# Optimization experiments

Measured on AMD Instinct MI355X. Metric: run time of the kernel, lower is better.

Reference implementation:

```python
import jax, jax.numpy as jnp
import numpy as np

EPS = 1e-5  # torch GroupNorm default


def setup_inputs() -> dict:
    key = jax.random.key(0)
    k1, k2, k3 = jax.random.split(key, 3)
    bs, l, dim = 16, 2048, 512
    G, varDim, numCodes = 2, 256, 320
    x = jax.random.normal(k1, (bs, l, dim), dtype=jnp.float32)
    # grouped 1x1 Conv1d weight: (groups, out_per_group, in_per_group)
    proj_w = jax.random.normal(k2, (G, varDim, varDim), dtype=jnp.float32) / np.sqrt(varDim)
    gn_weight = jnp.ones((dim,), dtype=jnp.float32)
    gn_bias = jnp.zeros((dim,), dtype=jnp.float32)
    embeddings = 0.01 * jax.random.normal(k3, (numCodes, 1, varDim), dtype=jnp.float32)
    return {"x": x, "proj_w": proj_w, "gn_weight": gn_weight,
            "gn_bias": gn_bias, "embeddings": embeddings}


def reference(x, proj_w, gn_weight, gn_bias, embeddings):
    bs, l, dim = x.shape
    G, varDim, _ = proj_w.shape
    numCodes = embeddings.shape[0]

    # --- projection: grouped 1x1 conv ---
    xg = x.transpose(0, 2, 1).reshape(bs, G, varDim, l)            # (bs,G,v,l)
    ze_g = jnp.einsum('gov,bgvl->bgol', proj_w, xg)                # (bs,G,v,l)

    # --- Fp32GroupNorm over (C/G * L) per group ---
    zf = ze_g.astype(jnp.float32)
    mean = zf.mean(axis=(2, 3), keepdims=True)
    var = zf.var(axis=(2, 3), keepdims=True)
    zn = (zf - mean) * jax.lax.rsqrt(var + EPS)
    ze = zn.reshape(bs, dim, l) * gn_weight[None, :, None] + gn_bias[None, :, None]
    ze = ze.astype(x.dtype)                                        # (bs,dim,l)

    # --- VQ: nearest code per group (argmin of L2 == argmin of sq dist) ---
    z = ze.reshape(bs, G, varDim, l).transpose(0, 3, 1, 2)         # (bs,l,G,v)
    emb = jnp.broadcast_to(embeddings, (numCodes, G, varDim))      # combineGroups expand
    dots = jnp.einsum('blgv,cgv->blgc', z, emb)                    # (bs,l,G,C)
    e2 = jnp.sum(emb * emb, axis=-1)                               # (C,G)
    dist = e2.T[None, None] - 2.0 * dots                           # ||z||^2 dropped: const over C
    idx = jnp.argmin(dist, axis=-1)                                # (bs,l,G)

    # gather codes per group
    zq = jnp.take_along_axis(
        emb.transpose(1, 0, 2)[None, None],                        # (1,1,G,C,v)
        idx[..., None, None], axis=3).squeeze(3)                   # (bs,l,G,v)
    zq = zq.reshape(bs, l, dim)

    # straight-through estimator; output shape (bs, l, dim)
    ze_bld = ze.transpose(0, 2, 1)
    out = jax.lax.stop_gradient(zq) + ze_bld - jax.lax.stop_gradient(ze_bld)
    return out
```

## Files before the change

### kernel.cpp

```cpp
#include <hip/hip_runtime.h>
#include <math.h>

typedef _Float16 half8_t  __attribute__((ext_vector_type(8)));
typedef _Float16 half4_t  __attribute__((ext_vector_type(4)));
typedef float    floatx16 __attribute__((ext_vector_type(16)));

#define BS   16
#define LL   2048
#define DIMC 512
#define NG   2
#define VD   256
#define NC   320
#define NELEM ((double)(VD*LL))

#define GLL(gsrc, ldst) __builtin_amdgcn_global_load_lds( \
    (const __attribute__((address_space(1))) unsigned int*)(gsrc), \
    (__attribute__((address_space(3))) unsigned int*)(ldst), 16, 0, 0)

#define MFMA32 __builtin_amdgcn_mfma_f32_32x32x16_f16

__global__ void k_prep(const float* __restrict__ W, const float* __restrict__ emb,
                       _Float16* __restrict__ Wimg, _Float16* __restrict__ Eimg,
                       float* __restrict__ e2f)
{
  const int blk = blockIdx.x, t = threadIdx.x;
  if (blk < 64) {
    int base = (blk * 256 + t) * 8;
    int k = base & 255, c = k >> 5, kk = k & 31;
    int row = (base >> 8) & 255, g = base >> 16;
    float4 v0 = *(const float4*)(W + base);
    float4 v1 = *(const float4*)(W + base + 4);
    float vv[8] = {v0.x, v0.y, v0.z, v0.w, v1.x, v1.y, v1.z, v1.w};
    half8_t hh, ll;
    #pragma unroll
    for (int i = 0; i < 8; ++i) {
      float s = vv[i] * 16.0f;
      _Float16 h = (_Float16)s;
      hh[i] = h; ll[i] = (_Float16)(s - (float)h);
    }
    size_t rb = ((size_t)(g * 8 + c) * 256 + row) * 72;
    *(half8_t*)&Wimg[rb + kk]      = hh;
    *(half8_t*)&Wimg[rb + 32 + kk] = ll;
  } else if (blk < 104) {
    int base = ((blk - 64) * 256 + t) * 8;
    int k = base & 255, c = k >> 5, kk = k & 31;
    int code = base >> 8;
    float4 v0 = *(const float4*)(emb + base);
    float4 v1 = *(const float4*)(emb + base + 4);
    float vv[8] = {v0.x, v0.y, v0.z, v0.w, v1.x, v1.y, v1.z, v1.w};
    half8_t hh, ll;
    #pragma unroll
    for (int i = 0; i < 8; ++i) {
      float s = vv[i] * 64.0f;
      _Float16 h = (_Float16)s;
      hh[i] = h; ll[i] = (_Float16)(s - (float)h);
    }
    size_t rb = ((size_t)c * 320 + code) * 72;
    *(half8_t*)&Eimg[rb + kk]      = hh;
    *(half8_t*)&Eimg[rb + 32 + kk] = ll;
  } else {
    int code = (blk - 104) * 256 + t;
    if (code < NC) {
      const float* er = emb + (size_t)code * VD;
      double s[4] = {0.0, 0.0, 0.0, 0.0};
      for (int v = 0; v < VD; v += 16)
        #pragma unroll
        for (int u = 0; u < 4; ++u) {
          float4 e4 = *(const float4*)(er + v + u * 4);
          s[u] += (double)e4.x * e4.x + (double)e4.y * e4.y
                + (double)e4.z * e4.z + (double)e4.w * e4.w;
        }
      e2f[code] = (float)(64.0 * (s[0] + s[1] + s[2] + s[3]));
    }
  }
}

__global__ __launch_bounds__(256, 2) void k_proj(
    const float* __restrict__ x, const _Float16* __restrict__ Wimg,
    float* __restrict__ ze, double* __restrict__ stats)
{
  __shared__ _Float16 Ah[128][72];
  __shared__ _Float16 Bh[256 * 72];

  const int blk = blockIdx.x;
  const int g  = blk & 1;
  const int m0 = (blk >> 1) * 128;
  const int b  = m0 >> 11;
  const int t  = threadIdx.x;
  const int lane = t & 63, w = t >> 6;
  const int col  = lane & 31, hq = lane >> 5;
  const int mw = (w & 1) * 64, nw = (w >> 1) * 128;

  const char* wbase = (const char*)(Wimg + (size_t)g * 8 * 256 * 72);

  floatx16 acc[2][4];
  #pragma unroll
  for (int i = 0; i < 2; ++i)
    #pragma unroll
    for (int j = 0; j < 4; ++j)
      #pragma unroll
      for (int e = 0; e < 16; ++e) acc[i][j][e] = 0.f;

  for (int c = 0; c < 8; ++c) {
    {
      const char* wc = wbase + (size_t)c * 256 * 144;
      #pragma unroll
      for (int i = 0; i < 9; ++i) {
        int off = (w * 9 + i) * 1024 + lane * 16;
        GLL(wc + off, (char*)Bh + off);
      }
    }
    #pragma unroll
    for (int i = 0; i < 4; ++i) {
      int idx = i * 256 + t;
      int row = idx >> 3, kq = idx & 7;
      float4 v = *(const float4*)(x + ((size_t)(m0 + row)) * DIMC + g * VD + c * 32 + kq * 4);
      half4_t hh, ll;
      { _Float16 h = (_Float16)v.x; hh[0] = h; ll[0] = (_Float16)(v.x - (float)h); }
      { _Float16 h = (_Float16)v.y; hh[1] = h; ll[1] = (_Float16)(v.y - (float)h); }
      { _Float16 h = (_Float16)v.z; hh[2] = h; ll[2] = (_Float16)(v.z - (float)h); }
      { _Float16 h = (_Float16)v.w; hh[3] = h; ll[3] = (_Float16)(v.w - (float)h); }
      *(half4_t*)&Ah[row][kq * 4]      = hh;
      *(half4_t*)&Ah[row][32 + kq * 4] = ll;
    }
    __syncthreads();
    #pragma unroll
    for (int ks = 0; ks < 2; ++ks) {
      const int ko = ks * 16 + hq * 8;
      half8_t azh[2], azl[2], bwh[4], bwl[4];
      #pragma unroll
      for (int i = 0; i < 2; ++i) {
        azh[i] = *(const half8_t*)&Ah[mw + i * 32 + col][ko];
        azl[i] = *(const half8_t*)&Ah[mw + i * 32 + col][32 + ko];
      }
      #pragma unroll
      for (int j = 0; j < 4; ++j) {
        bwh[j] = *(const half8_t*)&Bh[(nw + j * 32 + col) * 72 + ko];
        bwl[j] = *(const half8_t*)&Bh[(nw + j * 32 + col) * 72 + 32 + ko];
      }
      #pragma unroll
      for (int mi = 0; mi < 2; ++mi)
        #pragma unroll
        for (int ni = 0; ni < 4; ++ni) {
          acc[mi][ni] = MFMA32(azh[mi], bwh[ni], acc[mi][ni], 0, 0, 0);
          acc[mi][ni] = MFMA32(azh[mi], bwl[ni], acc[mi][ni], 0, 0, 0);
          acc[mi][ni] = MFMA32(azl[mi], bwh[ni], acc[mi][ni], 0, 0, 0);
        }
    }
    __syncthreads();
  }

  double s1 = 0.0, s2 = 0.0;
  #pragma unroll
  for (int mi = 0; mi < 2; ++mi)
    #pragma unroll
    for (int ni = 0; ni < 4; ++ni)
      #pragma unroll
      for (int r = 0; r < 16; ++r) {
        float vv = acc[mi][ni][r] * 0.0625f;
        double d = (double)vv; s1 += d; s2 += d * d;
        int ml = mw + mi * 32 + (r & 3) + 8 * (r >> 2) + 4 * hq;
        int nl = nw + ni * 32 + col;
        ze[((size_t)(m0 + ml)) * DIMC + g * VD + nl] = vv;
      }
  #pragma unroll
  for (int off = 32; off > 0; off >>= 1) {
    s1 += __shfl_down(s1, off);
    s2 += __shfl_down(s2, off);
  }
  if (lane == 0) {
    atomicAdd(&stats[(b * NG + g) * 2 + 0], s1);
    atomicAdd(&stats[(b * NG + g) * 2 + 1], s2);
  }
}

__global__ __launch_bounds__(256, 2) void k_vq(
    float* __restrict__ zio, const float* __restrict__ emb,
    const _Float16* __restrict__ Eimg,
    const float* __restrict__ gnw, const float* __restrict__ gnb,
    const double* __restrict__ stats, const float* __restrict__ e2f)
{
  __shared__ _Float16 Zs[128][72];
  __shared__ _Float16 Es[320 * 72];
  __shared__ float e2sh[NC];
  __shared__ int   idxs[128];
  __shared__ float cndv[2][128];
  __shared__ int   cndi[2][128];

  const int blk = blockIdx.x;
  const int g  = blk & 1;
  const int m0 = (blk >> 1) * 128;
  const int b  = m0 >> 11;
  const int t  = threadIdx.x;
  const int lane = t & 63, w = t >> 6;
  const int col  = lane & 31, hq = lane >> 5;
  const int ph = w & 1;
  const int mh = w >> 1;

  const int si = b * NG + g;
  double ss1 = stats[2 * si], ss2 = stats[2 * si + 1];
  double mu = ss1 / NELEM, var = ss2 / NELEM - mu * mu;
  const float mean = (float)mu;
  const float rstd = (float)(1.0 / sqrt(var + 1e-5));

  for (int c = t; c < NC; c += 256) e2sh[c] = e2f[c];

  float* zbase = zio + (size_t)m0 * DIMC + g * VD;
  const float* gw = gnw + g * VD;
  const float* gb = gnb + g * VD;

  floatx16 acc[5][2];
  #pragma unroll
  for (int i = 0; i < 5; ++i)
    #pragma unroll
    for (int f = 0; f < 2; ++f)
      #pragma unroll
      for (int e = 0; e < 16; ++e) acc[i][f][e] = 0.f;

  for (int c = 0; c < 8; ++c) {
    {
      const char* ec = (const char*)Eimg + (size_t)c * 320 * 144;
      for (int i = w; i < 45; i += 4) {
        int off = i * 1024 + lane * 16;
        GLL(ec + off, (char*)Es + off);
      }
    }
    #pragma unroll
    for (int i = 0; i < 4; ++i) {
      int idx = i * 256 + t;
      int row = idx >> 3, kq = idx & 7;
      float4 v  = *(const float4*)(zbase + (size_t)row * DIMC + c * 32 + kq * 4);
      float4 w4 = *(const float4*)(gw + c * 32 + kq * 4);
      float4 b4 = *(const float4*)(gb + c * 32 + kq * 4);
      float zn0 = (v.x - mean) * rstd * w4.x + b4.x;
      float zn1 = (v.y - mean) * rstd * w4.y + b4.y;
      float zn2 = (v.z - mean) * rstd * w4.z + b4.z;
      float zn3 = (v.w - mean) * rstd * w4.w + b4.w;
      half4_t hh, ll;
      { _Float16 h = (_Float16)zn0; hh[0] = h; ll[0] = (_Float16)(zn0 - (float)h); }
      { _Float16 h = (_Float16)zn1; hh[1] = h; ll[1] = (_Float16)(zn1 - (float)h); }
      { _Float16 h = (_Float16)zn2; hh[2] = h; ll[2] = (_Float16)(zn2 - (float)h); }
      { _Float16 h = (_Float16)zn3; hh[3] = h; ll[3] = (_Float16)(zn3 - (float)h); }
      *(half4_t*)&Zs[row][kq * 4]      = hh;
      *(half4_t*)&Zs[row][32 + kq * 4] = ll;
    }
    __syncthreads();
    #pragma unroll
    for (int ks = 0; ks < 2; ++ks) {
      const int ko = ks * 16 + hq * 8;
      half8_t bzh[2], bzl[2];
      #pragma unroll
      for (int f = 0; f < 2; ++f) {
        bzh[f] = *(const half8_t*)&Zs[ph * 64 + f * 32 + col][ko];
        bzl[f] = *(const half8_t*)&Zs[ph * 64 + f * 32 + col][32 + ko];
      }
      #pragma unroll
      for (int mtl = 0; mtl < 5; ++mtl) {
        const _Float16* erow = &Es[((mh * 5 + mtl) * 32 + col) * 72];
        half8_t aeh = *(const half8_t*)&erow[ko];
        half8_t ael = *(const half8_t*)&erow[32 + ko];
        #pragma unroll
        for (int f = 0; f < 2; ++f) {
          acc[mtl][f] = MFMA32(aeh, bzh[f], acc[mtl][f], 0, 0, 0);
          acc[mtl][f] = MFMA32(aeh, bzl[f], acc[mtl][f], 0, 0, 0);
          acc[mtl][f] = MFMA32(ael, bzh[f], acc[mtl][f], 0, 0, 0);
        }
      }
    }
    __syncthreads();
  }

  float bv0 = 3.4e38f, bv1 = 3.4e38f;
  int   bi0 = 0x7fffffff, bi1 = 0x7fffffff;
  #pragma unroll
  for (int mtl = 0; mtl < 5; ++mtl)
    #pragma unroll
    for (int r = 0; r < 16; ++r) {
      int code = (mh * 5 + mtl) * 32 + (r & 3) + 8 * (r >> 2) + 4 * hq;
      float d0 = e2sh[code] - 2.0f * acc[mtl][0][r];
      if (d0 < bv0 || (d0 == bv0 && code < bi0)) { bv0 = d0; bi0 = code; }
      float d1 = e2sh[code] - 2.0f * acc[mtl][1][r];
      if (d1 < bv1 || (d1 == bv1 && code < bi1)) { bv1 = d1; bi1 = code; }
    }
  {
    float ov = __shfl_xor(bv0, 32); int oi = __shfl_xor(bi0, 32);
    if (ov < bv0 || (ov == bv0 && oi < bi0)) { bv0 = ov; bi0 = oi; }
    ov = __shfl_xor(bv1, 32); oi = __shfl_xor(bi1, 32);
    if (ov < bv1 || (ov == bv1 && oi < bi1)) { bv1 = ov; bi1 = oi; }
  }
  if (hq == 0) {
    cndv[mh][ph * 64 + col]      = bv0; cndi[mh][ph * 64 + col]      = bi0;
    cndv[mh][ph * 64 + 32 + col] = bv1; cndi[mh][ph * 64 + 32 + col] = bi1;
  }
  __syncthreads();
  if (t < 128) {
    float v0 = cndv[0][t], v1 = cndv[1][t];
    int   i0 = cndi[0][t], i1 = cndi[1][t];
    idxs[t] = (v1 < v0 || (v1 == v0 && i1 < i0)) ? i1 : i0;
  }
  __syncthreads();

  #pragma unroll
  for (int it = 0; it < 32; ++it) {
    int idx = it * 256 + t;
    int row = idx >> 6, q4 = (idx & 63) * 4;
    int id = idxs[row];
    float4 e4 = *(const float4*)(emb + (size_t)id * VD + q4);
    *(float4*)(zbase + (size_t)row * DIMC + q4) = e4;
  }
}

extern "C" void kernel_launch(void* const* d_in, const int* in_sizes, int n_in,
                              void* d_out, int out_size, void* d_ws, size_t ws_size,
                              hipStream_t stream) {
  const float* x   = (const float*)d_in[0];
  const float* W   = (const float*)d_in[1];
  const float* gnw = (const float*)d_in[2];
  const float* gnb = (const float*)d_in[3];
  const float* emb = (const float*)d_in[4];
  float* out = (float*)d_out;

  double*   stats = (double*)d_ws;
  float*    e2f   = (float*)((char*)d_ws + 512);
  _Float16* Wimg  = (_Float16*)((char*)d_ws + 2048);
  _Float16* Eimg  = (_Float16*)((char*)d_ws + 591872);

  hipMemsetAsync(d_ws, 0, 512, stream);
  k_prep<<<106, 256, 0, stream>>>(W, emb, Wimg, Eimg, e2f);
  k_proj<<<512, 256, 0, stream>>>(x, Wimg, out, stats);
  k_vq<<<512, 256, 0, stream>>>(out, emb, Eimg, gnw, gnb, stats, e2f);
}
```

Measured before the change: 197.0 us.

## Double-buffer LDS tiles and use 512-thread blocks in proj and VQ kernels

After: 230.4 us. 16.9% more time.

```diff
diff --git a/kernel.cpp b/kernel.cpp
--- a/kernel.cpp
+++ b/kernel.cpp
@@ -75,12 +75,12 @@
   }
 }
 
-__global__ __launch_bounds__(256, 2) void k_proj(
+__global__ __launch_bounds__(512, 1) void k_proj(
     const float* __restrict__ x, const _Float16* __restrict__ Wimg,
     float* __restrict__ ze, double* __restrict__ stats)
 {
-  __shared__ _Float16 Ah[128][72];
-  __shared__ _Float16 Bh[256 * 72];
+  __shared__ _Float16 Ah[2][128][72];
+  __shared__ _Float16 Bh[2][256 * 72];
 
   const int blk = blockIdx.x;
   const int g  = blk & 1;
@@ -89,78 +89,99 @@
   const int t  = threadIdx.x;
   const int lane = t & 63, w = t >> 6;
   const int col  = lane & 31, hq = lane >> 5;
-  const int mw = (w & 1) * 64, nw = (w >> 1) * 128;
+  const int pw = (w & 1) * 64, ow = (w >> 1) * 64;
+  const int rw = t >> 3, kq = t & 7;
 
   const char* wbase = (const char*)(Wimg + (size_t)g * 8 * 256 * 72);
-
-  floatx16 acc[2][4];
+  const float* xrow = x + (size_t)m0 * DIMC + g * VD + kq * 4;
+
+  floatx16 acc[2][2];
   #pragma unroll
   for (int i = 0; i < 2; ++i)
     #pragma unroll
-    for (int j = 0; j < 4; ++j)
+    for (int j = 0; j < 2; ++j)
       #pragma unroll
       for (int e = 0; e < 16; ++e) acc[i][j][e] = 0.f;
 
+  for (int i = w; i < 36; i += 8) {
+    int off = i * 1024 + lane * 16;
+    GLL(wbase + off, (char*)Bh[0] + off);
+  }
+  #pragma unroll
+  for (int i = 0; i < 2; ++i) {
+    int row = i * 64 + rw;
+    float4 v = *(const float4*)(xrow + (size_t)row * DIMC);
+    half4_t hh, ll;
+    { _Float16 h = (_Float16)v.x; hh[0] = h; ll[0] = (_Float16)(v.x - (float)h); }
+    { _Float16 h = (_Float16)v.y; hh[1] = h; ll[1] = (_Float16)(v.y - (float)h); }
+    { _Float16 h = (_Float16)v.z; hh[2] = h; ll[2] = (_Float16)(v.z - (float)h); }
+    { _Float16 h = (_Float16)v.w; hh[3] = h; ll[3] = (_Float16)(v.w - (float)h); }
+    *(half4_t*)&Ah[0][row][kq * 4]      = hh;
+    *(half4_t*)&Ah[0][row][32 + kq * 4] = ll;
+  }
+
   for (int c = 0; c < 8; ++c) {
-    {
-      const char* wc = wbase + (size_t)c * 256 * 144;
-      #pragma unroll
-      for (int i = 0; i < 9; ++i) {
-        int off = (w * 9 + i) * 1024 + lane * 16;
-        GLL(wc + off, (char*)Bh + off);
-      }
-    }
-    #pragma unroll
-    for (int i = 0; i < 4; ++i) {
-      int idx = i * 256 + t;
-      int row = idx >> 3, kq = idx & 7;
-      float4 v = *(const float4*)(x + ((size_t)(m0 + row)) * DIMC + g * VD + c * 32 + kq * 4);
-      half4_t hh, ll;
-      { _Float16 h = (_Float16)v.x; hh[0] = h; ll[0] = (_Float16)(v.x - (float)h); }
-      { _Float16 h = (_Float16)v.y; hh[1] = h; ll[1] = (_Float16)(v.y - (float)h); }
-      { _Float16 h = (_Float16)v.z; hh[2] = h; ll[2] = (_Float16)(v.z - (float)h); }
-      { _Float16 h = (_Float16)v.w; hh[3] = h; ll[3] = (_Float16)(v.w - (float)h); }
-      *(half4_t*)&Ah[row][kq * 4]      = hh;
-      *(half4_t*)&Ah[row][32 + kq * 4] = ll;
-    }
     __syncthreads();
+    const int cur = c & 1, nxt = cur ^ 1;
+    if (c < 7) {
+      const char* wc = wbase + (size_t)(c + 1) * 256 * 144;
+      for (int i = w; i < 36; i += 8) {
+        int off = i * 1024 + lane * 16;
+        GLL(wc + off, (char*)Bh[nxt] + off);
+      }
+    }
+    float4 xv[2];
+    if (c < 7) {
+      #pragma unroll
+      for (int i = 0; i < 2; ++i)
+        xv[i] = *(const float4*)(xrow + (size_t)(i * 64 + rw) * DIMC + (c + 1) * 32);
+    }
     #pragma unroll
     for (int ks = 0; ks < 2; ++ks) {
       const int ko = ks * 16 + hq * 8;
-      half8_t azh[2], azl[2], bwh[4], bwl[4];
+      half8_t azh[2], azl[2], bwh[2], bwl[2];
       #pragma unroll
       for (int i = 0; i < 2; ++i) {
-        azh[i] = *(const half8_t*)&Ah[mw + i * 32 + col][ko];
-        azl[i] = *(const half8_t*)&Ah[mw + i * 32 + col][32 + ko];
-      }
-      #pragma unroll
-      for (int j = 0; j < 4; ++j) {
-        bwh[j] = *(const half8_t*)&Bh[(nw + j * 32 + col) * 72 + ko];
-        bwl[j] = *(const half8_t*)&Bh[(nw + j * 32 + col) * 72 + 32 + ko];
+        azh[i] = *(const half8_t*)&Ah[cur][pw + i * 32 + col][ko];
+        azl[i] = *(const half8_t*)&Ah[cur][pw + i * 32 + col][32 + ko];
+        bwh[i] = *(const half8_t*)&Bh[cur][(ow + i * 32 + col) * 72 + ko];
+        bwl[i] = *(const half8_t*)&Bh[cur][(ow + i * 32 + col) * 72 + 32 + ko];
       }
       #pragma unroll
       for (int mi = 0; mi < 2; ++mi)
         #pragma unroll
-        for (int ni = 0; ni < 4; ++ni) {
+        for (int ni = 0; ni < 2; ++ni) {
           acc[mi][ni] = MFMA32(azh[mi], bwh[ni], acc[mi][ni], 0, 0, 0);
           acc[mi][ni] = MFMA32(azh[mi], bwl[ni], acc[mi][ni], 0, 0, 0);
           acc[mi][ni] = MFMA32(azl[mi], bwh[ni], acc[mi][ni], 0, 0, 0);
         }
     }
-    __syncthreads();
+    if (c < 7) {
+      #pragma unroll
+      for (int i = 0; i < 2; ++i) {
+        int row = i * 64 + rw;
+        half4_t hh, ll;
+        { _Float16 h = (_Float16)xv[i].x; hh[0] = h; ll[0] = (_Float16)(xv[i].x - (float)h); }
+        { _Float16 h = (_Float16)xv[i].y; hh[1] = h; ll[1] = (_Float16)(xv[i].y - (float)h); }
+        { _Float16 h = (_Float16)xv[i].z; hh[2] = h; ll[2] = (_Float16)(xv[i].z - (float)h); }
+        { _Float16 h = (_Float16)xv[i].w; hh[3] = h; ll[3] = (_Float16)(xv[i].w - (float)h); }
+        *(half4_t*)&Ah[nxt][row][kq * 4]      = hh;
+        *(half4_t*)&Ah[nxt][row][32 + kq * 4] = ll;
+      }
+    }
   }
 
   double s1 = 0.0, s2 = 0.0;
   #pragma unroll
   for (int mi = 0; mi < 2; ++mi)
     #pragma unroll
-    for (int ni = 0; ni < 4; ++ni)
+    for (int ni = 0; ni < 2; ++ni)
       #pragma unroll
       for (int r = 0; r < 16; ++r) {
         float vv = acc[mi][ni][r] * 0.0625f;
         double d = (double)vv; s1 += d; s2 += d * d;
-        int ml = mw + mi * 32 + (r & 3) + 8 * (r >> 2) + 4 * hq;
-        int nl = nw + ni * 32 + col;
+        int ml = pw + mi * 32 + (r & 3) + 8 * (r >> 2) + 4 * hq;
+        int nl = ow + ni * 32 + col;
         ze[((size_t)(m0 + ml)) * DIMC + g * VD + nl] = vv;
       }
   #pragma unroll
@@ -174,14 +195,14 @@
   }
 }
 
-__global__ __launch_bounds__(256, 2) void k_vq(
+__global__ __launch_bounds__(512, 1) void k_vq(
     float* __restrict__ zio, const float* __restrict__ emb,
     const _Float16* __restrict__ Eimg,
     const float* __restrict__ gnw, const float* __restrict__ gnb,
     const double* __restrict__ stats, const float* __restrict__ e2f)
 {
-  __shared__ _Float16 Zs[128][72];
-  __shared__ _Float16 Es[320 * 72];
+  __shared__ _Float16 Zs[2][128][72];
+  __shared__ _Float16 Es[2][320 * 72];
   __shared__ float e2sh[NC];
   __shared__ int   idxs[128];
   __shared__ float cndv[2][128];
@@ -194,8 +215,9 @@
   const int t  = threadIdx.x;
   const int lane = t & 63, w = t >> 6;
   const int col  = lane & 31, hq = lane >> 5;
-  const int ph = w & 1;
-  const int mh = w >> 1;
+  const int ph = (w & 3) * 32;
+  const int mh = (w >> 2) * 5;
+  const int rw = t >> 3, kq = t & 7;
 
   const int si = b * NG + g;
   double ss1 = stats[2 * si], ss2 = stats[2 * si + 1];
@@ -203,94 +225,112 @@
   const float mean = (float)mu;
   const float rstd = (float)(1.0 / sqrt(var + 1e-5));
 
-  for (int c = t; c < NC; c += 256) e2sh[c] = e2f[c];
+  for (int cc = t; cc < NC; cc += 512) e2sh[cc] = e2f[cc];
 
   float* zbase = zio + (size_t)m0 * DIMC + g * VD;
+  const float* zrow = zbase + kq * 4;
   const float* gw = gnw + g * VD;
   const float* gb = gnb + g * VD;
 
-  floatx16 acc[5][2];
+  floatx16 acc[5];
   #pragma unroll
   for (int i = 0; i < 5; ++i)
     #pragma unroll
-    for (int f = 0; f < 2; ++f)
-      #pragma unroll
-      for (int e = 0; e < 16; ++e) acc[i][f][e] = 0.f;
-
-  for (int c = 0; c < 8; ++c) {
-    {
-      const char* ec = (const char*)Eimg + (size_t)c * 320 * 144;
-      for (int i = w; i < 45; i += 4) {
-        int off = i * 1024 + lane * 16;
-        GLL(ec + off, (char*)Es + off);
-      }
-    }
-    #pragma unroll
-    for (int i = 0; i < 4; ++i) {
-      int idx = i * 256 + t;
-      int row = idx >> 3, kq = idx & 7;
-      float4 v  = *(const float4*)(zbase + (size_t)row * DIMC + c * 32 + kq * 4);
-      float4 w4 = *(const float4*)(gw + c * 32 + kq * 4);
-      float4 b4 = *(const float4*)(gb + c * 32 + kq * 4);
-      float zn0 = (v.x - mean) * rstd * w4.x + b4.x;
-      float zn1 = (v.y - mean) * rstd * w4.y + b4.y;
-      float zn2 = (v.z - mean) * rstd * w4.z + b4.z;
-      float zn3 = (v.w - mean) * rstd * w4.w + b4.w;
+    for (int e = 0; e < 16; ++e) acc[i][e] = 0.f;
+
+  for (int i = w; i < 45; i += 8) {
+    int off = i * 1024 + lane * 16;
+    GLL((const char*)Eimg + off, (char*)Es[0] + off);
+  }
+  {
+    float4 wv = *(const float4*)(gw + kq * 4);
+    float4 bv = *(const float4*)(gb + kq * 4);
+    #pragma unroll
+    for (int i = 0; i < 2; ++i) {
+      int row = i * 64 + rw;
+      float4 v = *(const float4*)(zrow + (size_t)row * DIMC);
+      float zn0 = (v.x - mean) * rstd * wv.x + bv.x;
+      float zn1 = (v.y - mean) * rstd * wv.y + bv.y;
+      float zn2 = (v.z - mean) * rstd * wv.z + bv.z;
+      float zn3 = (v.w - mean) * rstd * wv.w + bv.w;
       half4_t hh, ll;
       { _Float16 h = (_Float16)zn0; hh[0] = h; ll[0] = (_Float16)(zn0 - (float)h); }
       { _Float16 h = (_Float16)zn1; hh[1] = h; ll[1] = (_Float16)(zn1 - (float)h); }
       { _Float16 h = (_Float16)zn2; hh[2] = h; ll[2] = (_Float16)(zn2 - (float)h); }
       { _Float16 h = (_Float16)zn3; hh[3] = h; ll[3] = (_Float16)(zn3 - (float)h); }
-      *(half4_t*)&Zs[row][kq * 4]      = hh;
-      *(half4_t*)&Zs[row][32 + kq * 4] = ll;
-    }
+      *(half4_t*)&Zs[0][row][kq * 4]      = hh;
+      *(half4_t*)&Zs[0][row][32 + kq * 4] = ll;
+    }
+  }
+
+  for (int c = 0; c < 8; ++c) {
     __syncthreads();
+    const int cur = c & 1, nxt = cur ^ 1;
+    if (c < 7) {
+      const char* ec = (const char*)Eimg + (size_t)(c + 1) * 320 * 144;
+      for (int i = w; i < 45; i += 8) {
+        int off = i * 1024 + lane * 16;
+        GLL(ec + off, (char*)Es[nxt] + off);
+      }
+    }
+    float4 zv[2], wv, bv;
+    if (c < 7) {
+      wv = *(const float4*)(gw + (c + 1) * 32 + kq * 4);
+      bv = *(const float4*)(gb + (c + 1) * 32 + kq * 4);
+      #pragma unroll
+      for (int i = 0; i < 2; ++i)
+        zv[i] = *(const float4*)(zrow + (size_t)(i * 64 + rw) * DIMC + (c + 1) * 32);
+    }
     #pragma unroll
     for (int ks = 0; ks < 2; ++ks) {
       const int ko = ks * 16 + hq * 8;
-      half8_t bzh[2], bzl[2];
-      #pragma unroll
-      for (int f = 0; f < 2; ++f) {
-        bzh[f] = *(const half8_t*)&Zs[ph * 64 + f * 32 + col][ko];
-        bzl[f] = *(const half8_t*)&Zs[ph * 64 + f * 32 + col][32 + ko];
-      }
+      half8_t bzh = *(const half8_t*)&Zs[cur][ph + col][ko];
+      half8_t bzl = *(const half8_t*)&Zs[cur][ph + col][32 + ko];
       #pragma unroll
       for (int mtl = 0; mtl < 5; ++mtl) {
-        const _Float16* erow = &Es[((mh * 5 + mtl) * 32 + col) * 72];
+        const _Float16* erow = &Es[cur][((mh + mtl) * 32 + col) * 72];
         half8_t aeh = *(const half8_t*)&erow[ko];
         half8_t ael = *(const half8_t*)&erow[32 + ko];
-        #pragma unroll
-        for (int f = 0; f < 2; ++f) {
-          acc[mtl][f] = MFMA32(aeh, bzh[f], acc[mtl][f], 0, 0, 0);
-          acc[mtl][f] = MFMA32(aeh, bzl[f], acc[mtl][f], 0, 0, 0);
-          acc[mtl][f] = MFMA32(ael, bzh[f], acc[mtl][f], 0, 0, 0);
-        }
-      }
-    }
-    __syncthreads();
-  }
-
-  float bv0 = 3.4e38f, bv1 = 3.4e38f;
-  int   bi0 = 0x7fffffff, bi1 = 0x7fffffff;
+        acc[mtl] = MFMA32(aeh, bzh, acc[mtl], 0, 0, 0);
+        acc[mtl] = MFMA32(aeh, bzl, acc[mtl], 0, 0, 0);
+        acc[mtl] = MFMA32(ael, bzh, acc[mtl], 0, 0, 0);
+      }
+    }
+    if (c < 7) {
+      #pragma unroll
+      for (int i = 0; i < 2; ++i) {
+        int row = i * 64 + rw;
+        float zn0 = (zv[i].x - mean) * rstd * wv.x + bv.x;
+        float zn1 = (zv[i].y - mean) * rstd * wv.y + bv.y;
+        float zn2 = (zv[i].z - mean) * rstd * wv.z + bv.z;
+        float zn3 = (zv[i].w - mean) * rstd * wv.w + bv.w;
+        half4_t hh, ll;
+        { _Float16 h = (_Float16)zn0; hh[0] = h; ll[0] = (_Float16)(zn0 - (float)h); }
+        { _Float16 h = (_Float16)zn1; hh[1] = h; ll[1] = (_Float16)(zn1 - (float)h); }
+        { _Float16 h = (_Float16)zn2; hh[2] = h; ll[2] = (_Float16)(zn2 - (float)h); }
+        { _Float16 h = (_Float16)zn3; hh[3] = h; ll[3] = (_Float16)(zn3 - (float)h); }
+        *(half4_t*)&Zs[nxt][row][kq * 4]      = hh;
+        *(half4_t*)&Zs[nxt][row][32 + kq * 4] = ll;
+      }
+    }
+  }
+
+  float bvv = 3.4e38f; int bii = 0x7fffffff;
   #pragma unroll
   for (int mtl = 0; mtl < 5; ++mtl)
     #pragma unroll
     for (int r = 0; r < 16; ++r) {
-      int code = (mh * 5 + mtl) * 32 + (r & 3) + 8 * (r >> 2) + 4 * hq;
-      float d0 = e2sh[code] - 2.0f * acc[mtl][0][r];
-      if (d0 < bv0 || (d0 == bv0 && code < bi0)) { bv0 = d0; bi0 = code; }
-      float d1 = e2sh[code] - 2.0f * acc[mtl][1][r];
-      if (d1 < bv1 || (d1 == bv1 && code < bi1)) { bv1 = d1; bi1 = code; }
+      int code = (mh + mtl) * 32 + (r & 3) + 8 * (r >> 2) + 4 * hq;
+      float d = e2sh[code] - 2.0f * acc[mtl][r];
+      if (d < bvv || (d == bvv && code < bii)) { bvv = d; bii = code; }
     }
   {
-    float ov = __shfl_xor(bv0, 32); int oi = __shfl_xor(bi0, 32);
-    if (ov < bv0 || (ov == bv0 && oi < bi0)) { bv0 = ov; bi0 = oi; }
-    ov = __shfl_xor(bv1, 32); oi = __shfl_xor(bi1, 32);
-    if (ov < bv1 || (ov == bv1 && oi < bi1)) { bv1 = ov; bi1 = oi; }
+    float ov = __shfl_xor(bvv, 32); int oi = __shfl_xor(bii, 32);
+    if (ov < bvv || (ov == bvv && oi < bii)) { bvv = ov; bii = oi; }
   }
   if (hq == 0) {
-    cndv[mh][ph * 64 + col]      = bv0; cndi[mh][ph * 64 + col]      = bi0;
-    cndv[mh][ph * 64 + 32 + col] = bv1; cndi[mh][ph * 64 + 32 + col] = bi1;
+    cndv[w >> 2][ph + col] = bvv;
+    cndi[w >> 2][ph + col] = bii;
   }
   __syncthreads();
   if (t < 128) {
@@ -301,8 +341,8 @@
   __syncthreads();
 
   #pragma unroll
-  for (int it = 0; it < 32; ++it) {
-    int idx = it * 256 + t;
+  for (int it = 0; it < 16; ++it) {
+    int idx = it * 512 + t;
     int row = idx >> 6, q4 = (idx & 63) * 4;
     int id = idxs[row];
     float4 e4 = *(const float4*)(emb + (size_t)id * VD + q4);
@@ -327,6 +367,6 @@
 
   hipMemsetAsync(d_ws, 0, 512, stream);
   k_prep<<<106, 256, 0, stream>>>(W, emb, Wimg, Eimg, e2f);
-  k_proj<<<512, 256, 0, stream>>>(x, Wimg, out, stats);
-  k_vq<<<512, 256, 0, stream>>>(out, emb, Eimg, gnw, gnb, stats, e2f);
+  k_proj<<<512, 512, 0, stream>>>(x, Wimg, out, stats);
+  k_vq<<<512, 512, 0, stream>>>(out, emb, Eimg, gnw, gnb, stats, e2f);
 }
```
